# Performance work log

Measured on AMD Instinct MI355X. Metric: run time of the kernel, lower is better.

The kernel has to match this reference:

```python
import jax, jax.numpy as jnp
import numpy as np

N = 300_000
DEG = 16
E = N * DEG
EPS_W = 1e-12  # guard for zero-distance neighbors
EPS_A = 1e-8   # diagonal regularization of the 3x3 normal matrix


def setup_inputs() -> dict:
    key = jax.random.key(0)
    k1, k2, k3 = jax.random.split(key, 3)
    coordinates = jax.random.normal(k1, (N, 3), dtype=jnp.float32)
    u = jax.random.normal(k2, (N, 1), dtype=jnp.float32)
    # uniform-degree CSR: offsets[i] = i*DEG
    offsets = (jnp.arange(N + 1) * DEG).astype(jnp.int32)
    indices = jax.random.randint(k3, (E,), 0, N, dtype=jnp.int32)
    return {"coordinates": coordinates, "u": u, "offsets": offsets, "indices": indices}


def _mesh_lsq_gradient(coords, values, offsets, indices):
    """Weighted least-squares gradient reconstruction over a CSR neighbor list.

    coords: [N,3], values: [N,C], offsets: [N+1], indices: [E].
    Returns [N,3,C]: per-node gradient of each channel.
    """
    n = coords.shape[0]
    e = indices.shape[0]
    # node id owning each edge: offsets[i] <= e < offsets[i+1]
    seg = jnp.searchsorted(offsets, jnp.arange(e, dtype=offsets.dtype), side='right') - 1
    dx = coords[indices] - coords[seg]            # [E,3]
    dv = values[indices] - values[seg]            # [E,C]
    w = 1.0 / jnp.maximum(jnp.sum(dx * dx, axis=-1), EPS_W)  # inverse-distance^2 weights [E]
    # normal equations: A g = b per node
    A = jax.ops.segment_sum(w[:, None, None] * dx[:, :, None] * dx[:, None, :], seg, num_segments=n)  # [N,3,3]
    b = jax.ops.segment_sum(w[:, None, None] * dx[:, :, None] * dv[:, None, :], seg, num_segments=n)  # [N,3,C]
    A = A + EPS_A * jnp.eye(3, dtype=coords.dtype)
    return jnp.linalg.solve(A, b)  # [N,3,C]


def reference(coordinates, u, offsets, indices):
    coords = jax.lax.stop_gradient(coordinates)  # original does coords.detach()
    vals = u[:, 0:1]                              # squeeze(-1), keep as 1 channel
    first = _mesh_lsq_gradient(coords, vals, offsets, indices)[..., 0]   # [N,3] = (u_x,u_y,u_z)
    # second pass: gradients of all three first derivatives at once (channels)
    second = _mesh_lsq_gradient(coords, first, offsets, indices)         # [N,3,3]; second[:,b,a] = d(du/dx_a)/dx_b
    u_xx = second[:, 0, 0]
    u_yy = second[:, 1, 1]
    u_zz = second[:, 2, 2]
    u_xy = second[:, 1, 0]  # mixed = second_grads[a][:, b] for a<b
    u_xz = second[:, 2, 0]
    u_yz = second[:, 2, 1]
    # columns: [xx, yy, zz, xy, xz, yz] (mixed derivs returned once; module duplicates symmetric keys)
    return jnp.stack([u_xx, u_yy, u_zz, u_xy, u_xz, u_yz], axis=-1)
```

## Files before the change

kernel.cpp:

```cpp
#include <hip/hip_runtime.h>


constexpr int N_NODES = 300000;
constexpr int DEG = 16;
constexpr float EPS_W = 1e-12f;
constexpr double EPS_A = 1e-8;

__device__ __forceinline__ float redux16(float v) {
    v += __shfl_xor(v, 1, 16);
    v += __shfl_xor(v, 2, 16);
    v += __shfl_xor(v, 4, 16);
    v += __shfl_xor(v, 8, 16);
    return v;
}

struct Adj3 {
    double j00, j01, j02, j11, j12, j22, inv;
};
__device__ __forceinline__ Adj3 adj3(float a00, float a01, float a02,
                                     float a11, float a12, float a22) {
    double A00 = (double)a00 + EPS_A;
    double A11 = (double)a11 + EPS_A;
    double A22 = (double)a22 + EPS_A;
    double A01 = (double)a01, A02 = (double)a02, A12 = (double)a12;
    Adj3 r;
    r.j00 = A11 * A22 - A12 * A12;
    r.j01 = A02 * A12 - A01 * A22;
    r.j02 = A01 * A12 - A02 * A11;
    r.j11 = A00 * A22 - A02 * A02;
    r.j12 = A01 * A02 - A00 * A12;
    r.j22 = A00 * A11 - A01 * A01;
    double det = A00 * r.j00 + A01 * r.j01 + A02 * r.j02;
    r.inv = 1.0 / det;
    return r;
}

__global__ __launch_bounds__(256) void pack_p1(
    const float* __restrict__ coords,
    const float* __restrict__ u,
    float4* __restrict__ p1)
{
    int i = blockIdx.x * 256 + threadIdx.x;
    if (i >= N_NODES) return;
    p1[i] = make_float4(coords[3 * i + 0], coords[3 * i + 1],
                        coords[3 * i + 2], u[i]);
}

__global__ __launch_bounds__(256) void lsq_pass1(
    const float4* __restrict__ p1,
    const int*    __restrict__ indices,
    float4*       __restrict__ p2)
{
    int tid  = blockIdx.x * 256 + threadIdx.x;
    int node = tid >> 4;
    int lane = tid & 15;
    if (node >= N_NODES) return;

    float4 c = p1[node];
    int j = __builtin_nontemporal_load(indices + node * DEG + lane);
    float4 p = p1[j];

    float dx = p.x - c.x, dy = p.y - c.y, dz = p.z - c.z, dv = p.w - c.w;
    float w = 1.0f / fmaxf(dx * dx + dy * dy + dz * dz, EPS_W);

    float a00 = redux16(w * dx * dx);
    float a01 = redux16(w * dx * dy);
    float a02 = redux16(w * dx * dz);
    float a11 = redux16(w * dy * dy);
    float a12 = redux16(w * dy * dz);
    float a22 = redux16(w * dz * dz);
    float b0  = redux16(w * dx * dv);
    float b1  = redux16(w * dy * dv);
    float b2  = redux16(w * dz * dv);

    if (lane == 0) {
        Adj3 s = adj3(a00, a01, a02, a11, a12, a22);
        float g0 = (float)((s.j00 * b0 + s.j01 * b1 + s.j02 * b2) * s.inv);
        float g1 = (float)((s.j01 * b0 + s.j11 * b1 + s.j12 * b2) * s.inv);
        float g2 = (float)((s.j02 * b0 + s.j12 * b1 + s.j22 * b2) * s.inv);
        p2[2 * node + 0] = make_float4(c.x, c.y, c.z, g0);
        p2[2 * node + 1] = make_float4(g1, g2, 0.0f, 0.0f);
    }
}

__global__ __launch_bounds__(256) void lsq_pass2(
    const float4* __restrict__ p2,
    const int*    __restrict__ indices,
    float*        __restrict__ out)
{
    int tid  = blockIdx.x * 256 + threadIdx.x;
    int node = tid >> 4;
    int lane = tid & 15;
    if (node >= N_NODES) return;

    float4 c0 = p2[2 * node + 0];
    float4 c1 = p2[2 * node + 1];
    int j = __builtin_nontemporal_load(indices + node * DEG + lane);
    float4 r0 = p2[2 * j + 0];
    float4 r1 = p2[2 * j + 1];

    float dx = r0.x - c0.x, dy = r0.y - c0.y, dz = r0.z - c0.z;
    float dv0 = r0.w - c0.w, dv1 = r1.x - c1.x, dv2 = r1.y - c1.y;
    float w = 1.0f / fmaxf(dx * dx + dy * dy + dz * dz, EPS_W);

    float a00 = redux16(w * dx * dx);
    float a01 = redux16(w * dx * dy);
    float a02 = redux16(w * dx * dz);
    float a11 = redux16(w * dy * dy);
    float a12 = redux16(w * dy * dz);
    float a22 = redux16(w * dz * dz);
    float b00 = redux16(w * dx * dv0);
    float b10 = redux16(w * dy * dv0);
    float b20 = redux16(w * dz * dv0);
    float b01 = redux16(w * dx * dv1);
    float b11 = redux16(w * dy * dv1);
    float b21 = redux16(w * dz * dv1);
    float b02 = redux16(w * dx * dv2);
    float b12 = redux16(w * dy * dv2);
    float b22 = redux16(w * dz * dv2);

    if (lane == 0) {
        Adj3 s = adj3(a00, a01, a02, a11, a12, a22);
        double x00 = (s.j00 * b00 + s.j01 * b10 + s.j02 * b20) * s.inv;
        double x10 = (s.j01 * b00 + s.j11 * b10 + s.j12 * b20) * s.inv;
        double x20 = (s.j02 * b00 + s.j12 * b10 + s.j22 * b20) * s.inv;
        double x11 = (s.j01 * b01 + s.j11 * b11 + s.j12 * b21) * s.inv;
        double x21 = (s.j02 * b01 + s.j12 * b11 + s.j22 * b21) * s.inv;
        double x22 = (s.j02 * b02 + s.j12 * b12 + s.j22 * b22) * s.inv;
        __builtin_nontemporal_store((float)x00, out + 6 * node + 0);
        __builtin_nontemporal_store((float)x11, out + 6 * node + 1);
        __builtin_nontemporal_store((float)x22, out + 6 * node + 2);
        __builtin_nontemporal_store((float)x10, out + 6 * node + 3);
        __builtin_nontemporal_store((float)x20, out + 6 * node + 4);
        __builtin_nontemporal_store((float)x21, out + 6 * node + 5);
    }
}

extern "C" void kernel_launch(void* const* d_in, const int* in_sizes, int n_in,
                              void* d_out, int out_size, void* d_ws, size_t ws_size,
                              hipStream_t stream) {
    const float* coords  = (const float*)d_in[0];
    const float* u       = (const float*)d_in[1];
    const int*   indices = (const int*)d_in[3];

    float4* p1 = (float4*)d_ws;
    float4* p2 = (float4*)((char*)d_ws + (size_t)N_NODES * 16);
    float*  out = (float*)d_out;

    const int threads = N_NODES * DEG;
    const int block = 256;
    const int grid_edges = (threads + block - 1) / block;
    const int grid_nodes = (N_NODES + block - 1) / block;

    pack_p1<<<grid_nodes, block, 0, stream>>>(coords, u, p1);
    lsq_pass1<<<grid_edges, block, 0, stream>>>(p1, indices, p2);
    lsq_pass2<<<grid_edges, block, 0, stream>>>(p2, indices, out);
}
```

Baseline: 166.1 us.

## Reuse pass-1 normal-matrix inverse and fp16 edge weights in second LSQ pass

Pass 1 now writes per-edge weighted offsets (w*dx, w*dy, w*dz) packed as fp16 and the per-node inverse of the 3x3 normal matrix, since both passes share the same geometry. Pass 2 then only gathers the 16-byte neighbor gradient instead of 32 bytes of coords plus gradients, skips the A-matrix reductions and the double-precision adjugate, and applies the stored inverse in fp32. The cost is an extra ~38 MB of per-edge workspace writes and reads, plus reduced precision from fp16 weights and the fp32 inverse. A fallback path keeps the old kernels when the workspace is too small.

```diff
diff --git a/kernel.cpp b/kernel.cpp
--- a/kernel.cpp
+++ b/kernel.cpp
@@ -1,10 +1,14 @@
 #include <hip/hip_runtime.h>
+#include <hip/hip_fp16.h>
 
 
 constexpr int N_NODES = 300000;
 constexpr int DEG = 16;
 constexpr float EPS_W = 1e-12f;
 constexpr double EPS_A = 1e-8;
+
+typedef float f32x4 __attribute__((ext_vector_type(4)));
+typedef float f32x2 __attribute__((ext_vector_type(2)));
 
 __device__ __forceinline__ float redux16(float v) {
     v += __shfl_xor(v, 1, 16);
@@ -14,27 +18,6 @@
     return v;
 }
 
-struct Adj3 {
-    double j00, j01, j02, j11, j12, j22, inv;
-};
-__device__ __forceinline__ Adj3 adj3(float a00, float a01, float a02,
-                                     float a11, float a12, float a22) {
-    double A00 = (double)a00 + EPS_A;
-    double A11 = (double)a11 + EPS_A;
-    double A22 = (double)a22 + EPS_A;
-    double A01 = (double)a01, A02 = (double)a02, A12 = (double)a12;
-    Adj3 r;
-    r.j00 = A11 * A22 - A12 * A12;
-    r.j01 = A02 * A12 - A01 * A22;
-    r.j02 = A01 * A12 - A02 * A11;
-    r.j11 = A00 * A22 - A02 * A02;
-    r.j12 = A01 * A02 - A00 * A12;
-    r.j22 = A00 * A11 - A01 * A01;
-    double det = A00 * r.j00 + A01 * r.j01 + A02 * r.j02;
-    r.inv = 1.0 / det;
-    return r;
-}
-
 __global__ __launch_bounds__(256) void pack_p1(
     const float* __restrict__ coords,
     const float* __restrict__ u,
@@ -46,7 +29,129 @@
                         coords[3 * i + 2], u[i]);
 }
 
-__global__ __launch_bounds__(256) void lsq_pass1(
+
+__global__ __launch_bounds__(256) void lsq_pass1_x(
+    const float4* __restrict__ p1,
+    const int*    __restrict__ indices,
+    float4*       __restrict__ G,
+    f32x4*        __restrict__ M,
+    f32x2*        __restrict__ WDX)
+{
+    int tid  = blockIdx.x * 256 + threadIdx.x;
+    int node = tid >> 4;
+    int lane = tid & 15;
+    if (node >= N_NODES) return;
+
+    float4 c = p1[node];
+    int e = node * DEG + lane;
+    int j = __builtin_nontemporal_load(indices + e);
+    float4 p = p1[j];
+
+    float dx = p.x - c.x, dy = p.y - c.y, dz = p.z - c.z, dv = p.w - c.w;
+    float w = 1.0f / fmaxf(dx * dx + dy * dy + dz * dz, EPS_W);
+    float wx = w * dx, wy = w * dy, wz = w * dz;
+
+    union { __half h[4]; f32x2 f2; } pk;
+    pk.h[0] = __float2half_rn(wx);
+    pk.h[1] = __float2half_rn(wy);
+    pk.h[2] = __float2half_rn(wz);
+    pk.h[3] = __float2half_rn(0.0f);
+    __builtin_nontemporal_store(pk.f2, WDX + e);
+
+    float a00 = redux16(wx * dx);
+    float a01 = redux16(wx * dy);
+    float a02 = redux16(wx * dz);
+    float a11 = redux16(wy * dy);
+    float a12 = redux16(wy * dz);
+    float a22 = redux16(wz * dz);
+    float b0  = redux16(wx * dv);
+    float b1  = redux16(wy * dv);
+    float b2  = redux16(wz * dv);
+
+    if (lane == 0) {
+        double A00 = (double)a00 + EPS_A;
+        double A11 = (double)a11 + EPS_A;
+        double A22 = (double)a22 + EPS_A;
+        double A01 = (double)a01, A02 = (double)a02, A12 = (double)a12;
+        double j00 = A11 * A22 - A12 * A12;
+        double j01 = A02 * A12 - A01 * A22;
+        double j02 = A01 * A12 - A02 * A11;
+        double j11 = A00 * A22 - A02 * A02;
+        double j12 = A01 * A02 - A00 * A12;
+        double j22 = A00 * A11 - A01 * A01;
+        double det = A00 * j00 + A01 * j01 + A02 * j02;
+        double inv = 1.0 / det;
+        float m00 = (float)(j00 * inv), m01 = (float)(j01 * inv);
+        float m02 = (float)(j02 * inv), m11 = (float)(j11 * inv);
+        float m12 = (float)(j12 * inv), m22 = (float)(j22 * inv);
+        float g0 = m00 * b0 + m01 * b1 + m02 * b2;
+        float g1 = m01 * b0 + m11 * b1 + m12 * b2;
+        float g2 = m02 * b0 + m12 * b1 + m22 * b2;
+        G[node] = make_float4(g0, g1, g2, 0.0f);
+        f32x4 mv0 = {m00, m01, m02, m11};
+        f32x4 mv1 = {m12, m22, 0.0f, 0.0f};
+        __builtin_nontemporal_store(mv0, M + 2 * node);
+        __builtin_nontemporal_store(mv1, M + 2 * node + 1);
+    }
+}
+
+__global__ __launch_bounds__(256) void lsq_pass2_x(
+    const float4* __restrict__ G,
+    const f32x4*  __restrict__ M,
+    const f32x2*  __restrict__ WDX,
+    const int*    __restrict__ indices,
+    float*        __restrict__ out)
+{
+    int tid  = blockIdx.x * 256 + threadIdx.x;
+    int node = tid >> 4;
+    int lane = tid & 15;
+    if (node >= N_NODES) return;
+
+    float4 gi = G[node];
+    int e = node * DEG + lane;
+    int j = __builtin_nontemporal_load(indices + e);
+    union { __half h[4]; f32x2 f2; } pk;
+    pk.f2 = __builtin_nontemporal_load(WDX + e);
+    float wx = __half2float(pk.h[0]);
+    float wy = __half2float(pk.h[1]);
+    float wz = __half2float(pk.h[2]);
+
+    float4 gj = G[j];
+    float dv0 = gj.x - gi.x, dv1 = gj.y - gi.y, dv2 = gj.z - gi.z;
+
+    float b00 = redux16(wx * dv0);
+    float b10 = redux16(wy * dv0);
+    float b20 = redux16(wz * dv0);
+    float b01 = redux16(wx * dv1);
+    float b11 = redux16(wy * dv1);
+    float b21 = redux16(wz * dv1);
+    float b02 = redux16(wx * dv2);
+    float b12 = redux16(wy * dv2);
+    float b22 = redux16(wz * dv2);
+
+    if (lane == 0) {
+        f32x4 m0 = __builtin_nontemporal_load(M + 2 * node);
+        f32x4 m1 = __builtin_nontemporal_load(M + 2 * node + 1);
+        float m00 = m0.x, m01 = m0.y, m02 = m0.z, m11 = m0.w;
+        float m12 = m1.x, m22 = m1.y;
+        float x00 = m00 * b00 + m01 * b10 + m02 * b20;
+        float x10 = m01 * b00 + m11 * b10 + m12 * b20;
+        float x20 = m02 * b00 + m12 * b10 + m22 * b20;
+        float x11 = m01 * b01 + m11 * b11 + m12 * b21;
+        float x21 = m02 * b01 + m12 * b11 + m22 * b21;
+        float x22 = m02 * b02 + m12 * b12 + m22 * b22;
+        f32x2* o2 = (f32x2*)(out + 6 * node);
+        f32x2 o0 = {x00, x11};
+        f32x2 o1 = {x22, x10};
+        f32x2 o2v = {x20, x21};
+        __builtin_nontemporal_store(o0, o2 + 0);
+        __builtin_nontemporal_store(o1, o2 + 1);
+        __builtin_nontemporal_store(o2v, o2 + 2);
+    }
+}
+
+
+__global__ __launch_bounds__(256) void lsq_pass1_fb(
     const float4* __restrict__ p1,
     const int*    __restrict__ indices,
     float4*       __restrict__ p2)
@@ -59,7 +164,6 @@
     float4 c = p1[node];
     int j = __builtin_nontemporal_load(indices + node * DEG + lane);
     float4 p = p1[j];
-
     float dx = p.x - c.x, dy = p.y - c.y, dz = p.z - c.z, dv = p.w - c.w;
     float w = 1.0f / fmaxf(dx * dx + dy * dy + dz * dz, EPS_W);
 
@@ -74,16 +178,27 @@
     float b2  = redux16(w * dz * dv);
 
     if (lane == 0) {
-        Adj3 s = adj3(a00, a01, a02, a11, a12, a22);
-        float g0 = (float)((s.j00 * b0 + s.j01 * b1 + s.j02 * b2) * s.inv);
-        float g1 = (float)((s.j01 * b0 + s.j11 * b1 + s.j12 * b2) * s.inv);
-        float g2 = (float)((s.j02 * b0 + s.j12 * b1 + s.j22 * b2) * s.inv);
+        double A00 = (double)a00 + EPS_A;
+        double A11 = (double)a11 + EPS_A;
+        double A22 = (double)a22 + EPS_A;
+        double A01 = (double)a01, A02 = (double)a02, A12 = (double)a12;
+        double j00 = A11 * A22 - A12 * A12;
+        double j01 = A02 * A12 - A01 * A22;
+        double j02 = A01 * A12 - A02 * A11;
+        double j11 = A00 * A22 - A02 * A02;
+        double j12 = A01 * A02 - A00 * A12;
+        double j22 = A00 * A11 - A01 * A01;
+        double det = A00 * j00 + A01 * j01 + A02 * j02;
+        double inv = 1.0 / det;
+        float g0 = (float)((j00 * b0 + j01 * b1 + j02 * b2) * inv);
+        float g1 = (float)((j01 * b0 + j11 * b1 + j12 * b2) * inv);
+        float g2 = (float)((j02 * b0 + j12 * b1 + j22 * b2) * inv);
         p2[2 * node + 0] = make_float4(c.x, c.y, c.z, g0);
         p2[2 * node + 1] = make_float4(g1, g2, 0.0f, 0.0f);
     }
 }
 
-__global__ __launch_bounds__(256) void lsq_pass2(
+__global__ __launch_bounds__(256) void lsq_pass2_fb(
     const float4* __restrict__ p2,
     const int*    __restrict__ indices,
     float*        __restrict__ out)
@@ -120,13 +235,24 @@
     float b22 = redux16(w * dz * dv2);
 
     if (lane == 0) {
-        Adj3 s = adj3(a00, a01, a02, a11, a12, a22);
-        double x00 = (s.j00 * b00 + s.j01 * b10 + s.j02 * b20) * s.inv;
-        double x10 = (s.j01 * b00 + s.j11 * b10 + s.j12 * b20) * s.inv;
-        double x20 = (s.j02 * b00 + s.j12 * b10 + s.j22 * b20) * s.inv;
-        double x11 = (s.j01 * b01 + s.j11 * b11 + s.j12 * b21) * s.inv;
-        double x21 = (s.j02 * b01 + s.j12 * b11 + s.j22 * b21) * s.inv;
-        double x22 = (s.j02 * b02 + s.j12 * b12 + s.j22 * b22) * s.inv;
+        double A00 = (double)a00 + EPS_A;
+        double A11 = (double)a11 + EPS_A;
+        double A22 = (double)a22 + EPS_A;
+        double A01 = (double)a01, A02 = (double)a02, A12 = (double)a12;
+        double j00 = A11 * A22 - A12 * A12;
+        double j01 = A02 * A12 - A01 * A22;
+        double j02 = A01 * A12 - A02 * A11;
+        double j11 = A00 * A22 - A02 * A02;
+        double j12 = A01 * A02 - A00 * A12;
+        double j22 = A00 * A11 - A01 * A01;
+        double det = A00 * j00 + A01 * j01 + A02 * j02;
+        double inv = 1.0 / det;
+        double x00 = (j00 * b00 + j01 * b10 + j02 * b20) * inv;
+        double x10 = (j01 * b00 + j11 * b10 + j12 * b20) * inv;
+        double x20 = (j02 * b00 + j12 * b10 + j22 * b20) * inv;
+        double x11 = (j01 * b01 + j11 * b11 + j12 * b21) * inv;
+        double x21 = (j02 * b01 + j12 * b11 + j22 * b21) * inv;
+        double x22 = (j02 * b02 + j12 * b12 + j22 * b22) * inv;
         __builtin_nontemporal_store((float)x00, out + 6 * node + 0);
         __builtin_nontemporal_store((float)x11, out + 6 * node + 1);
         __builtin_nontemporal_store((float)x22, out + 6 * node + 2);
@@ -142,17 +268,31 @@
     const float* coords  = (const float*)d_in[0];
     const float* u       = (const float*)d_in[1];
     const int*   indices = (const int*)d_in[3];
-
-    float4* p1 = (float4*)d_ws;
-    float4* p2 = (float4*)((char*)d_ws + (size_t)N_NODES * 16);
-    float*  out = (float*)d_out;
-
-    const int threads = N_NODES * DEG;
+    float*       out     = (float*)d_out;
+
     const int block = 256;
-    const int grid_edges = (threads + block - 1) / block;
+    const int grid_edges = (N_NODES * DEG) / block;
     const int grid_nodes = (N_NODES + block - 1) / block;
 
+    const size_t szP1  = (size_t)N_NODES * 16;
+    const size_t szG   = (size_t)N_NODES * 16;
+    const size_t szM   = (size_t)N_NODES * 32;
+    const size_t szWDX = (size_t)N_NODES * DEG * 8;
+    const size_t need_main = szP1 + szG + szM + szWDX;
+
+    char* ws = (char*)d_ws;
+    float4* p1 = (float4*)ws;
     pack_p1<<<grid_nodes, block, 0, stream>>>(coords, u, p1);
-    lsq_pass1<<<grid_edges, block, 0, stream>>>(p1, indices, p2);
-    lsq_pass2<<<grid_edges, block, 0, stream>>>(p2, indices, out);
-}
+
+    if (ws_size >= need_main) {
+        float4* G   = (float4*)(ws + szP1);
+        f32x4*  M   = (f32x4*)(ws + szP1 + szG);
+        f32x2*  WDX = (f32x2*)(ws + szP1 + szG + szM);
+        lsq_pass1_x<<<grid_edges, block, 0, stream>>>(p1, indices, G, M, WDX);
+        lsq_pass2_x<<<grid_edges, block, 0, stream>>>(G, M, WDX, indices, out);
+    } else {
+        float4* p2 = (float4*)(ws + szP1);
+        lsq_pass1_fb<<<grid_edges, block, 0, stream>>>(p1, indices, p2);
+        lsq_pass2_fb<<<grid_edges, block, 0, stream>>>(p2, indices, out);
+    }
+}
```

New measurement: 160.8 us. -3.2%, faster.

## Cache per-edge fp16 weights and inverse normal matrix for second pass

Applied to the files above, without the earlier changes.

Each node now uses 4 threads with 4 edges per thread and vectorized index loads, in place of 16 threads with one edge each, which shortens the shuffle reductions. Pass 1 stores the per-edge weighted offsets (w*dx, w*dy, w*dz) as fp16 and the inverted 3x3 matrix per node. Pass 2 therefore gathers only 16 bytes of gradient per neighbour and skips rebuilding and inverting A. The cost is extra streaming writes and reads of about 18 bytes per edge, plus fp16 rounding of the weights, which may hurt accuracy for near-coincident neighbours.

```diff
diff --git a/kernel.cpp b/kernel.cpp
--- a/kernel.cpp
+++ b/kernel.cpp
@@ -1,4 +1,5 @@
 #include <hip/hip_runtime.h>
+#include <hip/hip_fp16.h>
 
 
 constexpr int N_NODES = 300000;
@@ -6,33 +7,22 @@
 constexpr float EPS_W = 1e-12f;
 constexpr double EPS_A = 1e-8;
 
-__device__ __forceinline__ float redux16(float v) {
-    v += __shfl_xor(v, 1, 16);
-    v += __shfl_xor(v, 2, 16);
-    v += __shfl_xor(v, 4, 16);
-    v += __shfl_xor(v, 8, 16);
+typedef float        f32x4 __attribute__((ext_vector_type(4)));
+typedef float        f32x2 __attribute__((ext_vector_type(2)));
+typedef int          i32x4 __attribute__((ext_vector_type(4)));
+typedef unsigned int u32x4 __attribute__((ext_vector_type(4)));
+typedef unsigned int u32x2 __attribute__((ext_vector_type(2)));
+
+__device__ __forceinline__ float redux4(float v) {
+    v += __shfl_xor(v, 1, 4);
+    v += __shfl_xor(v, 2, 4);
     return v;
 }
 
-struct Adj3 {
-    double j00, j01, j02, j11, j12, j22, inv;
-};
-__device__ __forceinline__ Adj3 adj3(float a00, float a01, float a02,
-                                     float a11, float a12, float a22) {
-    double A00 = (double)a00 + EPS_A;
-    double A11 = (double)a11 + EPS_A;
-    double A22 = (double)a22 + EPS_A;
-    double A01 = (double)a01, A02 = (double)a02, A12 = (double)a12;
-    Adj3 r;
-    r.j00 = A11 * A22 - A12 * A12;
-    r.j01 = A02 * A12 - A01 * A22;
-    r.j02 = A01 * A12 - A02 * A11;
-    r.j11 = A00 * A22 - A02 * A02;
-    r.j12 = A01 * A02 - A00 * A12;
-    r.j22 = A00 * A11 - A01 * A01;
-    double det = A00 * r.j00 + A01 * r.j01 + A02 * r.j02;
-    r.inv = 1.0 / det;
-    return r;
+__device__ __forceinline__ unsigned int pack_h2(float a, float b) {
+    union { __half2 h2; unsigned int ui; } pk;
+    pk.h2 = __halves2half2(__float2half_rn(a), __float2half_rn(b));
+    return pk.ui;
 }
 
 __global__ __launch_bounds__(256) void pack_p1(
@@ -42,97 +32,151 @@
 {
     int i = blockIdx.x * 256 + threadIdx.x;
     if (i >= N_NODES) return;
-    p1[i] = make_float4(coords[3 * i + 0], coords[3 * i + 1],
+    p1[i] = make_float4(coords[3 * i], coords[3 * i + 1],
                         coords[3 * i + 2], u[i]);
 }
 
 __global__ __launch_bounds__(256) void lsq_pass1(
-    const float4* __restrict__ p1,
-    const int*    __restrict__ indices,
-    float4*       __restrict__ p2)
+    const float4*  __restrict__ P,
+    const int*     __restrict__ indices,
+    float4*        __restrict__ G,
+    f32x4*         __restrict__ M,
+    unsigned int*  __restrict__ WXY,
+    unsigned int*  __restrict__ WZ)
 {
     int tid  = blockIdx.x * 256 + threadIdx.x;
-    int node = tid >> 4;
-    int lane = tid & 15;
+    int node = tid >> 2;
+    int q    = tid & 3;
     if (node >= N_NODES) return;
 
-    float4 c = p1[node];
-    int j = __builtin_nontemporal_load(indices + node * DEG + lane);
-    float4 p = p1[j];
-
-    float dx = p.x - c.x, dy = p.y - c.y, dz = p.z - c.z, dv = p.w - c.w;
-    float w = 1.0f / fmaxf(dx * dx + dy * dy + dz * dz, EPS_W);
-
-    float a00 = redux16(w * dx * dx);
-    float a01 = redux16(w * dx * dy);
-    float a02 = redux16(w * dx * dz);
-    float a11 = redux16(w * dy * dy);
-    float a12 = redux16(w * dy * dz);
-    float a22 = redux16(w * dz * dz);
-    float b0  = redux16(w * dx * dv);
-    float b1  = redux16(w * dy * dv);
-    float b2  = redux16(w * dz * dv);
-
-    if (lane == 0) {
-        Adj3 s = adj3(a00, a01, a02, a11, a12, a22);
-        float g0 = (float)((s.j00 * b0 + s.j01 * b1 + s.j02 * b2) * s.inv);
-        float g1 = (float)((s.j01 * b0 + s.j11 * b1 + s.j12 * b2) * s.inv);
-        float g2 = (float)((s.j02 * b0 + s.j12 * b1 + s.j22 * b2) * s.inv);
-        p2[2 * node + 0] = make_float4(c.x, c.y, c.z, g0);
-        p2[2 * node + 1] = make_float4(g1, g2, 0.0f, 0.0f);
+    float4 c = P[node];
+    int ebase = node * DEG + q * 4;
+    i32x4 idx = __builtin_nontemporal_load((const i32x4*)(indices + ebase));
+
+    float4 n0 = P[idx.x];
+    float4 n1 = P[idx.y];
+    float4 n2 = P[idx.z];
+    float4 n3 = P[idx.w];
+
+    float a00 = 0, a01 = 0, a02 = 0, a11 = 0, a12 = 0, a22 = 0;
+    float b0 = 0, b1 = 0, b2 = 0;
+    float wxs[4], wys[4], wzs[4];
+    float4 nb[4] = {n0, n1, n2, n3};
+    #pragma unroll
+    for (int k = 0; k < 4; ++k) {
+        float dx = nb[k].x - c.x, dy = nb[k].y - c.y;
+        float dz = nb[k].z - c.z, dv = nb[k].w - c.w;
+        float w = 1.0f / fmaxf(dx * dx + dy * dy + dz * dz, EPS_W);
+        float wx = w * dx, wy = w * dy, wz = w * dz;
+        wxs[k] = wx; wys[k] = wy; wzs[k] = wz;
+        a00 += wx * dx; a01 += wx * dy; a02 += wx * dz;
+        a11 += wy * dy; a12 += wy * dz; a22 += wz * dz;
+        b0 += wx * dv; b1 += wy * dv; b2 += wz * dv;
+    }
+
+    u32x4 wxy = { pack_h2(wxs[0], wys[0]), pack_h2(wxs[1], wys[1]),
+                  pack_h2(wxs[2], wys[2]), pack_h2(wxs[3], wys[3]) };
+    __builtin_nontemporal_store(wxy, (u32x4*)(WXY + ebase));
+    u32x2 wzp = { pack_h2(wzs[0], wzs[1]), pack_h2(wzs[2], wzs[3]) };
+    __builtin_nontemporal_store(wzp, (u32x2*)(WZ + (ebase >> 1)));
+
+    a00 = redux4(a00); a01 = redux4(a01); a02 = redux4(a02);
+    a11 = redux4(a11); a12 = redux4(a12); a22 = redux4(a22);
+    b0 = redux4(b0); b1 = redux4(b1); b2 = redux4(b2);
+
+    if (q == 0) {
+        double A00 = (double)a00 + EPS_A;
+        double A11 = (double)a11 + EPS_A;
+        double A22 = (double)a22 + EPS_A;
+        double A01 = (double)a01, A02 = (double)a02, A12 = (double)a12;
+        double j00 = A11 * A22 - A12 * A12;
+        double j01 = A02 * A12 - A01 * A22;
+        double j02 = A01 * A12 - A02 * A11;
+        double j11 = A00 * A22 - A02 * A02;
+        double j12 = A01 * A02 - A00 * A12;
+        double j22 = A00 * A11 - A01 * A01;
+        double det = A00 * j00 + A01 * j01 + A02 * j02;
+        double inv = 1.0 / det;
+        float m00 = (float)(j00 * inv), m01 = (float)(j01 * inv);
+        float m02 = (float)(j02 * inv), m11 = (float)(j11 * inv);
+        float m12 = (float)(j12 * inv), m22 = (float)(j22 * inv);
+        G[node] = make_float4(m00 * b0 + m01 * b1 + m02 * b2,
+                              m01 * b0 + m11 * b1 + m12 * b2,
+                              m02 * b0 + m12 * b1 + m22 * b2, 0.0f);
+        f32x4 mv0 = {m00, m01, m02, m11};
+        f32x4 mv1 = {m12, m22, 0.0f, 0.0f};
+        __builtin_nontemporal_store(mv0, M + 2 * node);
+        __builtin_nontemporal_store(mv1, M + 2 * node + 1);
     }
 }
 
 __global__ __launch_bounds__(256) void lsq_pass2(
-    const float4* __restrict__ p2,
-    const int*    __restrict__ indices,
-    float*        __restrict__ out)
+    const float4*       __restrict__ G,
+    const f32x4*        __restrict__ M,
+    const unsigned int* __restrict__ WXY,
+    const unsigned int* __restrict__ WZ,
+    const int*          __restrict__ indices,
+    float*              __restrict__ out)
 {
     int tid  = blockIdx.x * 256 + threadIdx.x;
-    int node = tid >> 4;
-    int lane = tid & 15;
+    int node = tid >> 2;
+    int q    = tid & 3;
     if (node >= N_NODES) return;
 
-    float4 c0 = p2[2 * node + 0];
-    float4 c1 = p2[2 * node + 1];
-    int j = __builtin_nontemporal_load(indices + node * DEG + lane);
-    float4 r0 = p2[2 * j + 0];
-    float4 r1 = p2[2 * j + 1];
-
-    float dx = r0.x - c0.x, dy = r0.y - c0.y, dz = r0.z - c0.z;
-    float dv0 = r0.w - c0.w, dv1 = r1.x - c1.x, dv2 = r1.y - c1.y;
-    float w = 1.0f / fmaxf(dx * dx + dy * dy + dz * dz, EPS_W);
-
-    float a00 = redux16(w * dx * dx);
-    float a01 = redux16(w * dx * dy);
-    float a02 = redux16(w * dx * dz);
-    float a11 = redux16(w * dy * dy);
-    float a12 = redux16(w * dy * dz);
-    float a22 = redux16(w * dz * dz);
-    float b00 = redux16(w * dx * dv0);
-    float b10 = redux16(w * dy * dv0);
-    float b20 = redux16(w * dz * dv0);
-    float b01 = redux16(w * dx * dv1);
-    float b11 = redux16(w * dy * dv1);
-    float b21 = redux16(w * dz * dv1);
-    float b02 = redux16(w * dx * dv2);
-    float b12 = redux16(w * dy * dv2);
-    float b22 = redux16(w * dz * dv2);
-
-    if (lane == 0) {
-        Adj3 s = adj3(a00, a01, a02, a11, a12, a22);
-        double x00 = (s.j00 * b00 + s.j01 * b10 + s.j02 * b20) * s.inv;
-        double x10 = (s.j01 * b00 + s.j11 * b10 + s.j12 * b20) * s.inv;
-        double x20 = (s.j02 * b00 + s.j12 * b10 + s.j22 * b20) * s.inv;
-        double x11 = (s.j01 * b01 + s.j11 * b11 + s.j12 * b21) * s.inv;
-        double x21 = (s.j02 * b01 + s.j12 * b11 + s.j22 * b21) * s.inv;
-        double x22 = (s.j02 * b02 + s.j12 * b12 + s.j22 * b22) * s.inv;
-        __builtin_nontemporal_store((float)x00, out + 6 * node + 0);
-        __builtin_nontemporal_store((float)x11, out + 6 * node + 1);
-        __builtin_nontemporal_store((float)x22, out + 6 * node + 2);
-        __builtin_nontemporal_store((float)x10, out + 6 * node + 3);
-        __builtin_nontemporal_store((float)x20, out + 6 * node + 4);
-        __builtin_nontemporal_store((float)x21, out + 6 * node + 5);
+    float4 gi = G[node];
+    int ebase = node * DEG + q * 4;
+    i32x4 idx = __builtin_nontemporal_load((const i32x4*)(indices + ebase));
+    u32x4 wxy = __builtin_nontemporal_load((const u32x4*)(WXY + ebase));
+    u32x2 wzp = __builtin_nontemporal_load((const u32x2*)(WZ + (ebase >> 1)));
+
+    float4 g0 = G[idx.x];
+    float4 g1 = G[idx.y];
+    float4 g2 = G[idx.z];
+    float4 g3 = G[idx.w];
+
+    float b00 = 0, b10 = 0, b20 = 0;
+    float b01 = 0, b11 = 0, b21 = 0;
+    float b02 = 0, b12 = 0, b22 = 0;
+    float4 gb[4] = {g0, g1, g2, g3};
+    unsigned int wzs[2] = {wzp.x, wzp.y};
+    unsigned int wxys[4] = {wxy.x, wxy.y, wxy.z, wxy.w};
+    #pragma unroll
+    for (int k = 0; k < 4; ++k) {
+        union { __half2 h2; unsigned int ui; } pk;
+        pk.ui = wxys[k];
+        float wx = __low2float(pk.h2);
+        float wy = __high2float(pk.h2);
+        union { __half2 h2; unsigned int ui; } pz;
+        pz.ui = wzs[k >> 1];
+        float wz = (k & 1) ? __high2float(pz.h2) : __low2float(pz.h2);
+        float dv0 = gb[k].x - gi.x, dv1 = gb[k].y - gi.y, dv2 = gb[k].z - gi.z;
+        b00 += wx * dv0; b10 += wy * dv0; b20 += wz * dv0;
+        b01 += wx * dv1; b11 += wy * dv1; b21 += wz * dv1;
+        b02 += wx * dv2; b12 += wy * dv2; b22 += wz * dv2;
+    }
+
+    b00 = redux4(b00); b10 = redux4(b10); b20 = redux4(b20);
+    b01 = redux4(b01); b11 = redux4(b11); b21 = redux4(b21);
+    b02 = redux4(b02); b12 = redux4(b12); b22 = redux4(b22);
+
+    if (q == 0) {
+        f32x4 m0 = __builtin_nontemporal_load(M + 2 * node);
+        f32x4 m1 = __builtin_nontemporal_load(M + 2 * node + 1);
+        float m00 = m0.x, m01 = m0.y, m02 = m0.z, m11 = m0.w;
+        float m12 = m1.x, m22 = m1.y;
+        float x00 = m00 * b00 + m01 * b10 + m02 * b20;
+        float x10 = m01 * b00 + m11 * b10 + m12 * b20;
+        float x20 = m02 * b00 + m12 * b10 + m22 * b20;
+        float x11 = m01 * b01 + m11 * b11 + m12 * b21;
+        float x21 = m02 * b01 + m12 * b11 + m22 * b21;
+        float x22 = m02 * b02 + m12 * b12 + m22 * b22;
+        f32x2* o2 = (f32x2*)(out + 6 * node);
+        f32x2 o0 = {x00, x11};
+        f32x2 o1 = {x22, x10};
+        f32x2 o2v = {x20, x21};
+        __builtin_nontemporal_store(o0,  o2 + 0);
+        __builtin_nontemporal_store(o1,  o2 + 1);
+        __builtin_nontemporal_store(o2v, o2 + 2);
     }
 }
 
@@ -142,17 +186,26 @@
     const float* coords  = (const float*)d_in[0];
     const float* u       = (const float*)d_in[1];
     const int*   indices = (const int*)d_in[3];
-
-    float4* p1 = (float4*)d_ws;
-    float4* p2 = (float4*)((char*)d_ws + (size_t)N_NODES * 16);
-    float*  out = (float*)d_out;
-
-    const int threads = N_NODES * DEG;
+    float*       out     = (float*)d_out;
+
+    char* ws = (char*)d_ws;
+    const size_t szP1  = (size_t)N_NODES * 16;
+    const size_t szG   = (size_t)N_NODES * 16;
+    const size_t szM   = (size_t)N_NODES * 32;
+    const size_t szWXY = (size_t)N_NODES * DEG * 4;
+
+    float4*       P1  = (float4*)ws;
+    float4*       G   = (float4*)(ws + szP1);
+    f32x4*        M   = (f32x4*)(ws + szP1 + szG);
+    unsigned int* WXY = (unsigned int*)(ws + szP1 + szG + szM);
+    unsigned int* WZ  = (unsigned int*)(ws + szP1 + szG + szM + szWXY);
+
     const int block = 256;
-    const int grid_edges = (threads + block - 1) / block;
     const int grid_nodes = (N_NODES + block - 1) / block;
-
-    pack_p1<<<grid_nodes, block, 0, stream>>>(coords, u, p1);
-    lsq_pass1<<<grid_edges, block, 0, stream>>>(p1, indices, p2);
-    lsq_pass2<<<grid_edges, block, 0, stream>>>(p2, indices, out);
-}
+    const int threads4 = N_NODES * 4;
+    const int grid4 = (threads4 + block - 1) / block;
+
+    pack_p1<<<grid_nodes, block, 0, stream>>>(coords, u, P1);
+    lsq_pass1<<<grid4, block, 0, stream>>>(P1, indices, G, M, WXY, WZ);
+    lsq_pass2<<<grid4, block, 0, stream>>>(G, M, WXY, WZ, indices, out);
+}
```

After: 151.2 us. -9.0%, faster.
